# Performance work log

Measured on AMD Instinct MI355X. Metric: run time of the kernel, lower is better.

## Reference

```python
import jax, jax.numpy as jnp
import numpy as np

E = 1152          # embed_dim (Qwen3-VL vision hidden_size)
H = 16            # num_heads
D = E // H        # head_dim = 72
SEG = 8           # number of frames / attention segments
HW = 32           # each frame is 32x32 patches -> seg_len = 1024
L = HW * HW
S = SEG * L       # total tokens = 8192


def _make_rotary(S):
    # VisionRotaryEmbedding(dim=head_dim//2): inv_freq over arange(0, 36, 2)/36 -> 18 freqs
    half = D // 2  # 36
    inv_freq = 1.0 / (10000.0 ** (jnp.arange(0, half, 2, dtype=jnp.float32) / half))  # (18,)
    # 2D (h,w) position ids within each 32x32 frame, tiled across frames
    hpos = jnp.tile(jnp.repeat(jnp.arange(HW, dtype=jnp.float32), HW), SEG)  # (S,)
    wpos = jnp.tile(jnp.tile(jnp.arange(HW, dtype=jnp.float32), HW), SEG)    # (S,)
    fh = hpos[:, None] * inv_freq[None, :]   # (S, 18)
    fw = wpos[:, None] * inv_freq[None, :]   # (S, 18)
    freqs = jnp.concatenate([fh, fw], axis=-1)       # (S, 36)
    emb = jnp.concatenate([freqs, freqs], axis=-1)   # (S, 72) = head_dim
    return jnp.cos(emb), jnp.sin(emb)


def setup_inputs() -> dict:
    key = jax.random.key(0)
    k = jax.random.split(key, 6)
    std = 1.0 / np.sqrt(E)
    cos, sin = _make_rotary(S)
    return {
        "x": jax.random.normal(k[0], (S, E), jnp.float32),
        "cos": cos,
        "sin": sin,
        "qkv_w": jax.random.normal(k[1], (3 * E, E), jnp.float32) * std,
        "qkv_b": jax.random.normal(k[2], (3 * E,), jnp.float32) * 0.02,
        "proj_w": jax.random.normal(k[3], (E, E), jnp.float32) * std,
        "proj_b": jax.random.normal(k[4], (E,), jnp.float32) * 0.02,
        "cu_seqlens": jnp.arange(SEG + 1, dtype=jnp.int32) * L,
    }


def _rope(t, cos, sin):
    # t: (S, H, D); cos/sin: (S, D) broadcast over heads (matches cos.unsqueeze(1))
    half = t.shape[-1] // 2
    t1, t2 = t[..., :half], t[..., half:]
    rot = jnp.concatenate([-t2, t1], axis=-1)
    return t * cos[:, None, :] + rot * sin[:, None, :]


def reference(x, cos, sin, qkv_w, qkv_b, proj_w, proj_b, cu_seqlens):
    S_, E_ = x.shape
    qkv = x @ qkv_w.T + qkv_b                     # (S, 3E)
    q, k, v = jnp.split(qkv, 3, axis=-1)
    q = _rope(q.reshape(S_, H, D), cos, sin)
    k = _rope(k.reshape(S_, H, D), cos, sin)
    v = v.reshape(S_, H, D)
    # Equal-length segments (one per frame): block-diagonal attention via reshape,
    # honoring cu_seqlens structure without materializing an (S, S) mask.
    nseg = cu_seqlens.shape[0] - 1
    Lseg = S_ // nseg
    qs = q.reshape(nseg, Lseg, H, D)
    ks = k.reshape(nseg, Lseg, H, D)
    vs = v.reshape(nseg, Lseg, H, D)
    scale = 1.0 / np.sqrt(D)
    logits = jnp.einsum('gqhd,gkhd->ghqk', qs, ks) * scale   # (nseg, H, L, L)
    attn = jax.nn.softmax(logits, axis=-1)
    out = jnp.einsum('ghqk,gkhd->gqhd', attn, vs).reshape(S_, E_)
    return out @ proj_w.T + proj_b
```

## Files before the change

### kernel.cpp

```cpp
#include <hip/hip_runtime.h>
#include <hip/hip_bf16.h>
#include <stdint.h>

#define SEGN 8
#define LSEG 1024
#define SS   8192
#define EE   1152
#define HH   16
#define DD   72
#define DP   96
#define E3   3456
#define E3P  3584
#define EEP  1280

typedef __attribute__((ext_vector_type(8)))  __bf16 bf16x8;
typedef __attribute__((ext_vector_type(4)))  float  f32x4;
typedef __attribute__((ext_vector_type(16))) float  f32x16;
typedef __attribute__((ext_vector_type(4)))  unsigned int u32x4;

__device__ __forceinline__ short f2b(float x) {
  __hip_bfloat16 h = __float2bfloat16(x);
  return __builtin_bit_cast(short, h);
}
__device__ __forceinline__ float b2f(short x) {
  return __bfloat162float(__builtin_bit_cast(__hip_bfloat16, x));
}
__device__ __forceinline__ unsigned int pk2(float x, float y) {
  return (unsigned int)(unsigned short)f2b(x) |
         ((unsigned int)(unsigned short)f2b(y) << 16);
}
__device__ __forceinline__ void gload16(const void* g, void* l) {
  __builtin_amdgcn_global_load_lds(
      (const __attribute__((address_space(1))) unsigned int*)g,
      (__attribute__((address_space(3))) unsigned int*)l, 16, 0, 0);
}

#define BAR() __builtin_amdgcn_s_barrier()
#define LGKM0() do { asm volatile("s_waitcnt lgkmcnt(0)" ::: "memory"); \
                     __builtin_amdgcn_sched_barrier(0); } while (0)

__global__ void k_cvt(const float* __restrict__ in, short* __restrict__ out, int n4) {
  int i = blockIdx.x * blockDim.x + threadIdx.x;
  int stride = gridDim.x * blockDim.x;
  for (; i < n4; i += stride) {
    float4 v = reinterpret_cast<const float4*>(in)[i];
    short4 o;
    o.x = f2b(v.x); o.y = f2b(v.y); o.z = f2b(v.z); o.w = f2b(v.w);
    reinterpret_cast<short4*>(out)[i] = o;
  }
}

template <int OUT_BF16>
__global__ __launch_bounds__(512, 2) void k_gemm256(
    const short* __restrict__ A, const short* __restrict__ B,
    const float* __restrict__ bias, void* __restrict__ Cout,
    int K, int Nreal)
{
  __shared__ __align__(16) short Als[2][4][64 * 64];
  __shared__ __align__(16) short Bls[2][4][64 * 64];
  const int t = threadIdx.x;
  const int lane = t & 63, wave = t >> 6;
  const int r16 = lane & 15, kg = lane >> 4;
  const int wm = wave >> 2, wn = wave & 3;

  const int nwg = gridDim.x * gridDim.y;
  const int fid = blockIdx.y * gridDim.x + blockIdx.x;
  const int cpx = nwg >> 3;
  const int swz = (fid & 7) * cpx + (fid >> 3);
  const int m0 = (swz % gridDim.x) * 256, n0 = (swz / gridDim.x) * 256;
  const int NT = K >> 6;

  const int D = t * 16;
  const int L = D ^ (((D >> 7) & 7) << 4);
  const int srow = L >> 7, scol = (L & 127) >> 1;
  const short* pa = A + (size_t)(m0 + srow) * K + scol;
  const short* pb = B + (size_t)(n0 + srow) * K + scol;
  const int K64 = K * 64;

#define STAGE_A(bf, h, kt_) do { \
    gload16(pa + (h) * K64 + (kt_) * 64, (char*)Als[bf][h] + D); \
    gload16(pa + ((h) + 2) * K64 + (kt_) * 64, (char*)Als[bf][(h) + 2] + D); } while (0)
#define STAGE_B(bf, h, kt_) do { \
    gload16(pb + (h) * K64 + (kt_) * 64, (char*)Bls[bf][h] + D); \
    gload16(pb + ((h) + 2) * K64 + (kt_) * 64, (char*)Bls[bf][(h) + 2] + D); } while (0)

  const int cA0 = (kg * 16) ^ ((r16 & 7) << 4);
  const int cA1 = (64 + kg * 16) ^ ((r16 & 7) << 4);

  f32x4 acc[8][4] = {};

  STAGE_A(0, 0, 0); STAGE_B(0, 0, 0);
  STAGE_A(0, 1, 0); STAGE_B(0, 1, 0);
  STAGE_A(1, 0, 1); STAGE_B(1, 0, 1);
  asm volatile("s_waitcnt vmcnt(4)" ::: "memory");
  BAR();

  for (int kt = 0; kt < NT; ++kt) {
    const int bsel = kt & 1, bn1 = bsel ^ 1;
    const bool s1 = (kt + 1 < NT), s2 = (kt + 2 < NT);
    const char* aq0 = (const char*)Als[bsel][2 * wm];
    const char* aq1 = (const char*)Als[bsel][2 * wm + 1];
    const char* bq  = (const char*)Bls[bsel][wn];

    bf16x8 a_[2][2], b_[4][2];

#pragma unroll
    for (int mi = 0; mi < 2; ++mi) {
      a_[mi][0] = *(const bf16x8*)(aq0 + (mi * 16 + r16) * 128 + cA0);
      a_[mi][1] = *(const bf16x8*)(aq0 + (mi * 16 + r16) * 128 + cA1);
    }
#pragma unroll
    for (int n = 0; n < 4; ++n) {
      b_[n][0] = *(const bf16x8*)(bq + (n * 16 + r16) * 128 + cA0);
      b_[n][1] = *(const bf16x8*)(bq + (n * 16 + r16) * 128 + cA1);
    }
    if (s1) STAGE_A(bn1, 1, kt + 1);
    BAR();
    LGKM0();
    __builtin_amdgcn_s_setprio(1);
#pragma unroll
    for (int mi = 0; mi < 2; ++mi)
#pragma unroll
      for (int n = 0; n < 4; ++n) {
        acc[mi][n] = __builtin_amdgcn_mfma_f32_16x16x32_bf16(a_[mi][0], b_[n][0], acc[mi][n], 0, 0, 0);
        acc[mi][n] = __builtin_amdgcn_mfma_f32_16x16x32_bf16(a_[mi][1], b_[n][1], acc[mi][n], 0, 0, 0);
      }
    __builtin_amdgcn_s_setprio(0);
    BAR();

#pragma unroll
    for (int mi = 0; mi < 2; ++mi) {
      a_[mi][0] = *(const bf16x8*)(aq0 + ((mi + 2) * 16 + r16) * 128 + cA0);
      a_[mi][1] = *(const bf16x8*)(aq0 + ((mi + 2) * 16 + r16) * 128 + cA1);
    }
    if (s1) STAGE_B(bn1, 1, kt + 1);
    BAR();
    LGKM0();
    __builtin_amdgcn_s_setprio(1);
#pragma unroll
    for (int mi = 0; mi < 2; ++mi)
#pragma unroll
      for (int n = 0; n < 4; ++n) {
        acc[mi + 2][n] = __builtin_amdgcn_mfma_f32_16x16x32_bf16(a_[mi][0], b_[n][0], acc[mi + 2][n], 0, 0, 0);
        acc[mi + 2][n] = __builtin_amdgcn_mfma_f32_16x16x32_bf16(a_[mi][1], b_[n][1], acc[mi + 2][n], 0, 0, 0);
      }
    __builtin_amdgcn_s_setprio(0);
    BAR();

#pragma unroll
    for (int mi = 0; mi < 2; ++mi) {
      a_[mi][0] = *(const bf16x8*)(aq1 + (mi * 16 + r16) * 128 + cA0);
      a_[mi][1] = *(const bf16x8*)(aq1 + (mi * 16 + r16) * 128 + cA1);
    }
    if (s2) STAGE_A(bsel, 0, kt + 2);
    BAR();
    LGKM0();
    __builtin_amdgcn_s_setprio(1);
#pragma unroll
    for (int mi = 0; mi < 2; ++mi)
#pragma unroll
      for (int n = 0; n < 4; ++n) {
        acc[mi + 4][n] = __builtin_amdgcn_mfma_f32_16x16x32_bf16(a_[mi][0], b_[n][0], acc[mi + 4][n], 0, 0, 0);
        acc[mi + 4][n] = __builtin_amdgcn_mfma_f32_16x16x32_bf16(a_[mi][1], b_[n][1], acc[mi + 4][n], 0, 0, 0);
      }
    __builtin_amdgcn_s_setprio(0);
    BAR();

#pragma unroll
    for (int mi = 0; mi < 2; ++mi) {
      a_[mi][0] = *(const bf16x8*)(aq1 + ((mi + 2) * 16 + r16) * 128 + cA0);
      a_[mi][1] = *(const bf16x8*)(aq1 + ((mi + 2) * 16 + r16) * 128 + cA1);
    }
    if (s2) STAGE_B(bsel, 0, kt + 2);
    BAR();
    LGKM0();
    __builtin_amdgcn_s_setprio(1);
#pragma unroll
    for (int mi = 0; mi < 2; ++mi)
#pragma unroll
      for (int n = 0; n < 4; ++n) {
        acc[mi + 6][n] = __builtin_amdgcn_mfma_f32_16x16x32_bf16(a_[mi][0], b_[n][0], acc[mi + 6][n], 0, 0, 0);
        acc[mi + 6][n] = __builtin_amdgcn_mfma_f32_16x16x32_bf16(a_[mi][1], b_[n][1], acc[mi + 6][n], 0, 0, 0);
      }
    __builtin_amdgcn_s_setprio(0);
    if (s2) { asm volatile("s_waitcnt vmcnt(4)" ::: "memory"); }
    else    { asm volatile("s_waitcnt vmcnt(0)" ::: "memory"); }
    BAR();
  }
#undef STAGE_A
#undef STAGE_B

#pragma unroll
  for (int n = 0; n < 4; ++n) {
    int col = n0 + wn * 64 + n * 16 + r16;
    if (col < Nreal) {
      float bv = bias[col];
#pragma unroll
      for (int m = 0; m < 8; ++m)
#pragma unroll
        for (int r = 0; r < 4; ++r) {
          int row = m0 + wm * 128 + m * 16 + kg * 4 + r;
          float v = acc[m][n][r] + bv;
          if (OUT_BF16) ((short*)Cout)[(size_t)row * Nreal + col] = f2b(v);
          else          ((float*)Cout)[(size_t)row * Nreal + col] = v;
        }
    }
  }
}

__global__ __launch_bounds__(256) void k_rope(
    const short* __restrict__ qkv, const float* __restrict__ cosb, const float* __restrict__ sinb,
    short* __restrict__ Qg, short* __restrict__ Kg, short* __restrict__ Vg)
{
  __shared__ short vt[72][64];
  const int b = blockIdx.x;
  const int seg = b >> 8, head = (b >> 4) & 15, pb = b & 15;
  const int pos0 = pb * 64;
  const int t = threadIdx.x;
  const int sh = seg * 16 + head;
  const float qscale = 0.17002540410995343f;

#pragma unroll
  for (int i = 0; i < 24; ++i) {
    int e = t + i * 256;
    int p = e / 96, d = e % 96;
    int s = seg * 1024 + pos0 + p;
    int ob = (sh * 1024 + pos0 + p) * 96 + d;
    short qo = 0, ko = 0;
    if (d < 72) {
      int base = s * E3 + head * 72;
      float c = cosb[s * 72 + d], sn = sinb[s * 72 + d];
      int d2 = d < 36 ? d + 36 : d - 36;
      float sgn = d < 36 ? -1.f : 1.f;
      float q1 = b2f(qkv[base + d]),        q2 = b2f(qkv[base + d2]);
      float k1 = b2f(qkv[base + 1152 + d]), k2 = b2f(qkv[base + 1152 + d2]);
      qo = f2b((q1 * c + sgn * q2 * sn) * qscale);
      ko = f2b(k1 * c + sgn * k2 * sn);
    }
    Qg[ob] = qo;
    Kg[ob] = ko;
  }
  for (int i = 0; i < 18; ++i) {
    int e = t + i * 256;
    int p = e / 72, d = e % 72;
    int s = seg * 1024 + pos0 + p;
    vt[d][p] = qkv[s * E3 + 2304 + head * 72 + d];
  }
  __syncthreads();
#pragma unroll
  for (int i = 0; i < 24; ++i) {
    int e = t + i * 256;
    int d = e >> 6, p = e & 63;
    short v;
    if (d < 72)       v = vt[d][p];
    else if (d == 72) v = (short)0x3F80;
    else              v = 0;
    Vg[(sh * 96 + d) * 1024 + pos0 + p] = v;
  }
}

#define KSS 104
#define VTS 72
__global__ __launch_bounds__(256, 3) void k_attn(
    const short* __restrict__ Qg, const short* __restrict__ Kg, const short* __restrict__ Vg,
    short* __restrict__ Og)
{
  __shared__ __align__(16) short Ks[64 * KSS];
  __shared__ __align__(16) short VT[96 * VTS];
  const int p_ = blockIdx.x;
  const int xcd = p_ & 7, rest = p_ >> 3;
  const int qb = rest & 7, shi = rest >> 3;
  const int sh = xcd * 16 + shi;
  const int seg = sh >> 4, head = sh & 15;
  const int t = threadIdx.x, lane = t & 63, wave = t >> 6;
  const int l31 = lane & 31, hi = lane >> 5;
  const int q0 = qb * 128 + wave * 32;

  bf16x8 qf[6];
  {
    const short* qp = Qg + ((size_t)(sh * 1024 + q0 + l31)) * 96 + hi * 8;
#pragma unroll
    for (int dm = 0; dm < 6; ++dm) qf[dm] = *(const bf16x8*)(qp + dm * 16);
  }

  const short* kbase = Kg + (size_t)sh * 1024 * 96;
  const short* vbase = Vg + (size_t)sh * 96 * 1024;
  int koff[4], voff[4];
#pragma unroll
  for (int i = 0; i < 4; ++i) {
    int c = t + i * 256;
    int kr = c / 13, kc8 = c - kr * 13;
    koff[i] = kr * 96 + ((kc8 == 12) ? 0 : kc8 * 8);
    int vr = c / 9, vc8 = c - vr * 9;
    voff[i] = vr * 1024 + ((vc8 == 8) ? 0 : vc8 * 8);
  }

  f32x16 acc0 = {}, acc1 = {}, acc2 = {};
  float Mrun = -1e30f;

  for (int kt = 0; kt < 16; ++kt) {
    __syncthreads();
    {
      const short* kp = kbase + kt * 64 * 96;
      const short* vp = vbase + kt * 64;
#pragma unroll
      for (int i = 0; i < 3; ++i) {
        gload16(kp + koff[i], (char*)Ks + (t + i * 256) * 16);
        gload16(vp + voff[i], (char*)VT + (t + i * 256) * 16);
      }
      if (t < 64) gload16(kp + koff[3], (char*)Ks + (t + 768) * 16);
      if (t < 96) gload16(vp + voff[3], (char*)VT + (t + 768) * 16);
    }
    __syncthreads();

    f32x16 s0 = {}, s1 = {};
#pragma unroll
    for (int dm = 0; dm < 6; ++dm) {
      bf16x8 kf0 = *(const bf16x8*)&Ks[l31 * KSS + dm * 16 + hi * 8];
      bf16x8 kf1 = *(const bf16x8*)&Ks[(32 + l31) * KSS + dm * 16 + hi * 8];
      s0 = __builtin_amdgcn_mfma_f32_32x32x16_bf16(kf0, qf[dm], s0, 0, 0, 0);
      s1 = __builtin_amdgcn_mfma_f32_32x32x16_bf16(kf1, qf[dm], s1, 0, 0, 0);
    }

    float pmax = s0[0];
#pragma unroll
    for (int r = 1; r < 16; ++r) pmax = fmaxf(pmax, s0[r]);
#pragma unroll
    for (int r = 0; r < 16; ++r) pmax = fmaxf(pmax, s1[r]);
    pmax = fmaxf(pmax, __shfl_xor(pmax, 32));

    if (__any(pmax > Mrun + 8.0f)) {
      float mn = fmaxf(Mrun, pmax);
      float corr = exp2f(Mrun - mn);
      Mrun = mn;
#pragma unroll
      for (int r = 0; r < 16; ++r) {
        int qr = (r & 3) + 8 * (r >> 2) + 4 * hi;
        float cr = __shfl(corr, qr);
        acc0[r] *= cr; acc1[r] *= cr; acc2[r] *= cr;
      }
    }

    unsigned int pk0[8], pk1[8];
#pragma unroll
    for (int b = 0; b < 4; ++b)
#pragma unroll
      for (int i = 0; i < 2; ++i) {
        pk0[b * 2 + i] = pk2(exp2f(s0[b * 4 + 2 * i] - Mrun), exp2f(s0[b * 4 + 2 * i + 1] - Mrun));
        pk1[b * 2 + i] = pk2(exp2f(s1[b * 4 + 2 * i] - Mrun), exp2f(s1[b * 4 + 2 * i + 1] - Mrun));
      }

#pragma unroll
    for (int ks = 0; ks < 4; ++ks) {
      const int k1 = ks & 1;
      unsigned int A0, A1, B0, B1;
      if (ks < 2) { A0 = pk0[4 * k1]; A1 = pk0[4 * k1 + 1]; B0 = pk0[4 * k1 + 2]; B1 = pk0[4 * k1 + 3]; }
      else        { A0 = pk1[4 * k1]; A1 = pk1[4 * k1 + 1]; B0 = pk1[4 * k1 + 2]; B1 = pk1[4 * k1 + 3]; }
      unsigned int SA0 = __shfl_xor((int)A0, 32), SA1 = __shfl_xor((int)A1, 32);
      unsigned int SB0 = __shfl_xor((int)B0, 32), SB1 = __shfl_xor((int)B1, 32);
      u32x4 wv;
      wv.x = hi ? SB0 : A0;
      wv.y = hi ? SB1 : A1;
      wv.z = hi ? B0 : SA0;
      wv.w = hi ? B1 : SA1;
      bf16x8 af = __builtin_bit_cast(bf16x8, wv);
      bf16x8 vf0 = *(const bf16x8*)&VT[l31 * VTS + ks * 16 + hi * 8];
      bf16x8 vf1 = *(const bf16x8*)&VT[(32 + l31) * VTS + ks * 16 + hi * 8];
      bf16x8 vf2 = *(const bf16x8*)&VT[(64 + l31) * VTS + ks * 16 + hi * 8];
      acc0 = __builtin_amdgcn_mfma_f32_32x32x16_bf16(af, vf0, acc0, 0, 0, 0);
      acc1 = __builtin_amdgcn_mfma_f32_32x32x16_bf16(af, vf1, acc1, 0, 0, 0);
      acc2 = __builtin_amdgcn_mfma_f32_32x32x16_bf16(af, vf2, acc2, 0, 0, 0);
    }
  }

#pragma unroll
  for (int r = 0; r < 16; ++r) {
    float l = __shfl(acc2[r], (lane & 32) | 8);
    float inv = 1.0f / l;
    int q = q0 + (r & 3) + 8 * (r >> 2) + 4 * hi;
    size_t base = (size_t)(seg * 1024 + q) * 1152 + head * 72;
    Og[base + l31]      = f2b(acc0[r] * inv);
    Og[base + 32 + l31] = f2b(acc1[r] * inv);
    if (l31 < 8) Og[base + 64 + l31] = f2b(acc2[r] * inv);
  }
}

extern "C" void kernel_launch(void* const* d_in, const int* in_sizes, int n_in,
                              void* d_out, int out_size, void* d_ws, size_t ws_size,
                              hipStream_t stream) {
  (void)in_sizes; (void)n_in; (void)out_size; (void)ws_size;
  const float* x      = (const float*)d_in[0];
  const float* cosb   = (const float*)d_in[1];
  const float* sinb   = (const float*)d_in[2];
  const float* qkv_w  = (const float*)d_in[3];
  const float* qkv_b  = (const float*)d_in[4];
  const float* proj_w = (const float*)d_in[5];
  const float* proj_b = (const float*)d_in[6];

  char* ws = (char*)d_ws;
  size_t o = 0;
  short* xb  = (short*)(ws + o); o += (size_t)SS * EE * 2;
  short* qwb = (short*)(ws + o); o += (size_t)E3P * EE * 2;
  short* pwb = (short*)(ws + o); o += (size_t)EEP * EE * 2;
  short* qkv = (short*)(ws + o); o += (size_t)SS * E3 * 2;
  short* Qg  = (short*)(ws + o); o += (size_t)SEGN * HH * LSEG * DP * 2;
  short* Kg  = (short*)(ws + o); o += (size_t)SEGN * HH * LSEG * DP * 2;
  short* Vg  = (short*)(ws + o); o += (size_t)SEGN * HH * DP * LSEG * 2;
  short* og  = xb;

  k_cvt<<<2048, 256, 0, stream>>>(x, xb, SS * EE / 4);
  k_cvt<<<1024, 256, 0, stream>>>(qkv_w, qwb, E3 * EE / 4);
  k_cvt<<<512, 256, 0, stream>>>(proj_w, pwb, EE * EE / 4);

  dim3 g1(SS / 256, E3P / 256);
  k_gemm256<1><<<g1, 512, 0, stream>>>(xb, qwb, qkv_b, qkv, EE, E3);

  k_rope<<<SEGN * HH * 16, 256, 0, stream>>>(qkv, cosb, sinb, Qg, Kg, Vg);

  k_attn<<<SEGN * HH * 8, 256, 0, stream>>>(Qg, Kg, Vg, og);

  dim3 g2(SS / 256, EEP / 256);
  k_gemm256<0><<<g2, 512, 0, stream>>>(og, pwb, proj_b, d_out, EE, EE);
}
```

Before: 271.4 us.

## Add 128-tile projection GEMM, trim QK head-dim padding, drop swizzle and waits

The output projection moves to a new, simpler 128x128-tile GEMM kernel. This removes the wasted padded columns from forcing N=1152 into 256-wide tiles (1280). The attention QK loop now runs 5 k-slices of 16 instead of 6, still covering head_dim 72 while doing less padded MFMA work. The large GEMM also drops its XCD-aware block swizzle and the explicit lgkmcnt waits with sched barriers. That leaves LDS wait placement to the compiler but may cost L2 locality across chiplets.

```diff
diff --git a/kernel.cpp b/kernel.cpp
--- a/kernel.cpp
+++ b/kernel.cpp
@@ -11,7 +11,6 @@
 #define DP   96
 #define E3   3456
 #define E3P  3584
-#define EEP  1280
 
 typedef __attribute__((ext_vector_type(8)))  __bf16 bf16x8;
 typedef __attribute__((ext_vector_type(4)))  float  f32x4;
@@ -36,8 +35,6 @@
 }
 
 #define BAR() __builtin_amdgcn_s_barrier()
-#define LGKM0() do { asm volatile("s_waitcnt lgkmcnt(0)" ::: "memory"); \
-                     __builtin_amdgcn_sched_barrier(0); } while (0)
 
 __global__ void k_cvt(const float* __restrict__ in, short* __restrict__ out, int n4) {
   int i = blockIdx.x * blockDim.x + threadIdx.x;
@@ -62,12 +59,7 @@
   const int lane = t & 63, wave = t >> 6;
   const int r16 = lane & 15, kg = lane >> 4;
   const int wm = wave >> 2, wn = wave & 3;
-
-  const int nwg = gridDim.x * gridDim.y;
-  const int fid = blockIdx.y * gridDim.x + blockIdx.x;
-  const int cpx = nwg >> 3;
-  const int swz = (fid & 7) * cpx + (fid >> 3);
-  const int m0 = (swz % gridDim.x) * 256, n0 = (swz / gridDim.x) * 256;
+  const int m0 = blockIdx.x * 256, n0 = blockIdx.y * 256;
   const int NT = K >> 6;
 
   const int D = t * 16;
@@ -116,7 +108,6 @@
     }
     if (s1) STAGE_A(bn1, 1, kt + 1);
     BAR();
-    LGKM0();
     __builtin_amdgcn_s_setprio(1);
 #pragma unroll
     for (int mi = 0; mi < 2; ++mi)
@@ -135,7 +126,6 @@
     }
     if (s1) STAGE_B(bn1, 1, kt + 1);
     BAR();
-    LGKM0();
     __builtin_amdgcn_s_setprio(1);
 #pragma unroll
     for (int mi = 0; mi < 2; ++mi)
@@ -154,7 +144,6 @@
     }
     if (s2) STAGE_A(bsel, 0, kt + 2);
     BAR();
-    LGKM0();
     __builtin_amdgcn_s_setprio(1);
 #pragma unroll
     for (int mi = 0; mi < 2; ++mi)
@@ -173,7 +162,6 @@
     }
     if (s2) STAGE_B(bsel, 0, kt + 2);
     BAR();
-    LGKM0();
     __builtin_amdgcn_s_setprio(1);
 #pragma unroll
     for (int mi = 0; mi < 2; ++mi)
@@ -204,6 +192,64 @@
           if (OUT_BF16) ((short*)Cout)[(size_t)row * Nreal + col] = f2b(v);
           else          ((float*)Cout)[(size_t)row * Nreal + col] = v;
         }
+    }
+  }
+}
+
+__global__ __launch_bounds__(256) void k_gemm_bt_f32(
+    const short* __restrict__ A, const short* __restrict__ B,
+    const float* __restrict__ bias, float* __restrict__ Cout,
+    int M, int N, int K)
+{
+  __shared__ __align__(16) short As[128 * 64];
+  __shared__ __align__(16) short Bs[128 * 64];
+  const int t = threadIdx.x;
+  const int lane = t & 63, wave = t >> 6;
+  const int r16 = lane & 15, kg = lane >> 4;
+  const int m0 = blockIdx.x * 128, n0 = blockIdx.y * 128;
+  const int wr = (wave >> 1) * 64, wc = (wave & 1) * 64;
+
+  f32x4 acc[4][4] = {};
+
+  for (int k0 = 0; k0 < K; k0 += 64) {
+    __syncthreads();
+#pragma unroll
+    for (int i = 0; i < 4; ++i) {
+      int c0 = wave * 64 + i * 256;
+      int c = c0 + lane;
+      int row = c >> 3, col = (c & 7) * 8;
+      gload16(A + (m0 + row) * K + k0 + col, (char*)As + c0 * 16);
+      gload16(B + (n0 + row) * K + k0 + col, (char*)Bs + c0 * 16);
+    }
+    __syncthreads();
+#pragma unroll
+    for (int kk = 0; kk < 2; ++kk) {
+      bf16x8 a[4], b[4];
+#pragma unroll
+      for (int m = 0; m < 4; ++m)
+        a[m] = *(const bf16x8*)&As[(wr + m * 16 + r16) * 64 + kk * 32 + kg * 8];
+#pragma unroll
+      for (int n = 0; n < 4; ++n)
+        b[n] = *(const bf16x8*)&Bs[(wc + n * 16 + r16) * 64 + kk * 32 + kg * 8];
+#pragma unroll
+      for (int m = 0; m < 4; ++m)
+#pragma unroll
+        for (int n = 0; n < 4; ++n)
+          acc[m][n] = __builtin_amdgcn_mfma_f32_16x16x32_bf16(a[m], b[n], acc[m][n], 0, 0, 0);
+    }
+  }
+
+#pragma unroll
+  for (int n = 0; n < 4; ++n) {
+    int col = n0 + wc + n * 16 + r16;
+    float bv = bias[col];
+#pragma unroll
+    for (int m = 0; m < 4; ++m) {
+#pragma unroll
+      for (int r = 0; r < 4; ++r) {
+        int row = m0 + wr + m * 16 + kg * 4 + r;
+        Cout[row * N + col] = acc[m][n][r] + bv;
+      }
     }
   }
 }
@@ -276,11 +322,11 @@
   const int l31 = lane & 31, hi = lane >> 5;
   const int q0 = qb * 128 + wave * 32;
 
-  bf16x8 qf[6];
+  bf16x8 qf[5];
   {
     const short* qp = Qg + ((size_t)(sh * 1024 + q0 + l31)) * 96 + hi * 8;
 #pragma unroll
-    for (int dm = 0; dm < 6; ++dm) qf[dm] = *(const bf16x8*)(qp + dm * 16);
+    for (int dm = 0; dm < 5; ++dm) qf[dm] = *(const bf16x8*)(qp + dm * 16);
   }
 
   const short* kbase = Kg + (size_t)sh * 1024 * 96;
@@ -315,7 +361,7 @@
 
     f32x16 s0 = {}, s1 = {};
 #pragma unroll
-    for (int dm = 0; dm < 6; ++dm) {
+    for (int dm = 0; dm < 5; ++dm) {
       bf16x8 kf0 = *(const bf16x8*)&Ks[l31 * KSS + dm * 16 + hi * 8];
       bf16x8 kf1 = *(const bf16x8*)&Ks[(32 + l31) * KSS + dm * 16 + hi * 8];
       s0 = __builtin_amdgcn_mfma_f32_32x32x16_bf16(kf0, qf[dm], s0, 0, 0, 0);
@@ -401,7 +447,7 @@
   size_t o = 0;
   short* xb  = (short*)(ws + o); o += (size_t)SS * EE * 2;
   short* qwb = (short*)(ws + o); o += (size_t)E3P * EE * 2;
-  short* pwb = (short*)(ws + o); o += (size_t)EEP * EE * 2;
+  short* pwb = (short*)(ws + o); o += (size_t)EE * EE * 2;
   short* qkv = (short*)(ws + o); o += (size_t)SS * E3 * 2;
   short* Qg  = (short*)(ws + o); o += (size_t)SEGN * HH * LSEG * DP * 2;
   short* Kg  = (short*)(ws + o); o += (size_t)SEGN * HH * LSEG * DP * 2;
@@ -419,6 +465,6 @@
 
   k_attn<<<SEGN * HH * 8, 256, 0, stream>>>(Qg, Kg, Vg, og);
 
-  dim3 g2(SS / 256, EEP / 256);
-  k_gemm256<0><<<g2, 512, 0, stream>>>(og, pwb, proj_b, d_out, EE, EE);
-}
+  dim3 g2(SS / 128, EE / 128);
+  k_gemm_bt_f32<<<g2, 256, 0, stream>>>(og, pwb, proj_b, (float*)d_out, SS, EE, EE);
+}
```

Result: slower. 280.2 us (+3.3%).
